# Optimization experiments

Hardware: AMD Instinct MI355X
Metric: run time of the kernel (lower is better)

Reference implementation:

```python
import jax, jax.numpy as jnp
import numpy as np
import math

B, S, D, H, FF, V, L = 8, 1024, 512, 8, 2048, 32000, 6
HD = D // H
EPS = 1e-6


def _positional_encoding(seq_len, d_model):
    pos = np.arange(seq_len, dtype=np.float32)[:, None]
    div = np.exp(np.arange(0, d_model, 2, dtype=np.float32) * (-math.log(10000.0) / d_model))
    pe = np.zeros((seq_len, d_model), dtype=np.float32)
    pe[:, 0::2] = np.sin(pos * div)
    pe[:, 1::2] = np.cos(pos * div)
    return jnp.asarray(pe)[None]  # [1, S, D]


def setup_inputs() -> dict:
    key = jax.random.key(0)
    ks = jax.random.split(key, 10)
    s = 0.02
    return {
        'tokens': jax.random.randint(ks[0], (B, S), 0, V, dtype=jnp.int32),
        'mask': jnp.ones((B, 1, 1, S), dtype=jnp.int32),
        'emb': jax.random.normal(ks[1], (V, D), jnp.float32) * s,
        'Wq': jax.random.normal(ks[2], (D, D), jnp.float32) * s,
        'bq': jnp.zeros((D,), jnp.float32),
        'Wk': jax.random.normal(ks[3], (D, D), jnp.float32) * s,
        'bk': jnp.zeros((D,), jnp.float32),
        'Wv': jax.random.normal(ks[4], (D, D), jnp.float32) * s,
        'bv': jnp.zeros((D,), jnp.float32),
        'Wo': jax.random.normal(ks[5], (D, D), jnp.float32) * s,
        'bo': jnp.zeros((D,), jnp.float32),
        'W1': jax.random.normal(ks[6], (D, FF), jnp.float32) * s,
        'b1': jnp.zeros((FF,), jnp.float32),
        'W2': jax.random.normal(ks[7], (FF, D), jnp.float32) * s,
        'b2': jnp.zeros((D,), jnp.float32),
        'ln_a1': jnp.ones((1,), jnp.float32),
        'ln_b1': jnp.zeros((1,), jnp.float32),
        'ln_a2': jnp.ones((1,), jnp.float32),
        'ln_b2': jnp.zeros((1,), jnp.float32),
    }


def _layernorm(x, alpha, bias):
    # custom LN from source: unbiased std (torch default), scalar alpha/bias,
    # eps added to std (not variance)
    mean = jnp.mean(x, axis=-1, keepdims=True)
    std = jnp.std(x, axis=-1, keepdims=True, ddof=1)
    return alpha * (x - mean) / (std + EPS) + bias


def reference(tokens, mask, emb, Wq, bq, Wk, bk, Wv, bv, Wo, bo,
              W1, b1, W2, b2, ln_a1, ln_b1, ln_a2, ln_b2):
    b, s = tokens.shape
    x = emb[tokens] * jnp.asarray(math.sqrt(D), emb.dtype)  # [B,S,D]
    x = x + _positional_encoding(s, D)
    neg = jnp.asarray(-1e9, x.dtype)
    scale = jnp.asarray(1.0 / math.sqrt(HD), x.dtype)
    # NOTE: source reuses the same EncoderBlock instance -> shared weights per layer
    for _ in range(L):
        # --- self-attention sublayer (pre-norm residual) ---
        h = _layernorm(x, ln_a1, ln_b1)
        q = (h @ Wq + bq).reshape(b, s, H, HD).transpose(0, 2, 1, 3)
        k = (h @ Wk + bk).reshape(b, s, H, HD).transpose(0, 2, 1, 3)
        v = (h @ Wv + bv).reshape(b, s, H, HD).transpose(0, 2, 1, 3)
        scores = jnp.einsum('bhqd,bhkd->bhqk', q, k) * scale
        scores = jnp.where(mask == 0, neg, scores)
        attn = jax.nn.softmax(scores, axis=-1)
        o = jnp.einsum('bhqk,bhkd->bhqd', attn, v)
        o = o.transpose(0, 2, 1, 3).reshape(b, s, D)
        x = x + (o @ Wo + bo)
        # --- feed-forward sublayer (pre-norm residual) ---
        h2 = _layernorm(x, ln_a2, ln_b2)
        x = x + (jax.nn.relu(h2 @ W1 + b1) @ W2 + b2)
    return x
```

## Files before the change

### kernel.cpp

```cpp
#include <hip/hip_runtime.h>
#include <hip/hip_bf16.h>
#include <math.h>

#define BB 8
#define SS 1024
#define DD 512
#define HH 8
#define FF 2048
#define LL 6
#define HD 64
#define MM (BB * SS)
#define EPS 1e-6f
#define QKVS 1536

typedef __attribute__((ext_vector_type(8))) short bf16x8;
typedef __attribute__((ext_vector_type(4))) float f32x4;

typedef __attribute__((address_space(1))) const unsigned int g_u32;
typedef __attribute__((address_space(3))) unsigned int l_u32;

__device__ __forceinline__ short f2bf(float f) {
    union { float f; unsigned u; } c; c.f = f;
    unsigned u = c.u;
    u += 0x7fff + ((u >> 16) & 1);
    return (short)(u >> 16);
}

__device__ __forceinline__ void gload_lds16(const void* g, void* l) {
    __builtin_amdgcn_global_load_lds((g_u32*)g, (l_u32*)l, 16, 0, 0);
}

#define SWZB(row, cb) (((row) * 128) + ((cb) ^ ((((row) & 7) ^ (((row) >> 3) & 7)) << 4)))

__global__ __launch_bounds__(256) void embed_pe_kernel(
    const int* __restrict__ tokens, const float* __restrict__ emb,
    float* __restrict__ x)
{
    int idx = blockIdx.x * 256 + threadIdx.x;
    int d  = idx & (DD - 1);
    int bs = idx >> 9;
    int s  = bs & (SS - 1);
    int tok = tokens[bs];
    float val = emb[(size_t)tok * DD + d] * 22.62741699796952f;
    int i2 = d & ~1;
    float freq = expf((float)i2 * -0.017988946039015984f);
    float ang = (float)s * freq;
    val += (d & 1) ? cosf(ang) : sinf(ang);
    x[idx] = val;
}

__global__ __launch_bounds__(256) void wcvt_kernel(
    const float* __restrict__ W, short* __restrict__ Wt, int K, int N)
{
    __shared__ float tile[32][33];
    int n0 = blockIdx.x * 32, k0 = blockIdx.y * 32;
    int tx = threadIdx.x & 31, ty = threadIdx.x >> 5;
    #pragma unroll
    for (int i = 0; i < 4; ++i)
        tile[ty + i * 8][tx] = W[(size_t)(k0 + ty + i * 8) * N + n0 + tx];
    __syncthreads();
    #pragma unroll
    for (int i = 0; i < 4; ++i)
        Wt[(size_t)(n0 + ty + i * 8) * K + k0 + tx] = f2bf(tile[tx][ty + i * 8]);
}

__global__ __launch_bounds__(256) void bcat_kernel(
    const float* __restrict__ bq, const float* __restrict__ bk,
    const float* __restrict__ bv, float* __restrict__ out)
{
    int i = blockIdx.x * 256 + threadIdx.x;
    float v = (i < 512) ? bq[i] : (i < 1024 ? bk[i - 512] : bv[i - 1024]);
    out[i] = v;
}

__global__ __launch_bounds__(256) void ln_kernel(
    const float* __restrict__ x, short* __restrict__ y,
    const float* __restrict__ alpha_p, const float* __restrict__ beta_p)
{
    int t = threadIdx.x;
    int half = t >> 7, i = t & 127;
    int row = blockIdx.x * 2 + half;
    const float* xr = x + (size_t)row * DD;
    float4 v = *(const float4*)(xr + i * 4);

    __shared__ float red[8];
    float s = v.x + v.y + v.z + v.w;
    #pragma unroll
    for (int o = 32; o >= 1; o >>= 1) s += __shfl_xor(s, o, 64);
    int wv = t >> 6;
    if ((t & 63) == 0) red[wv] = s;
    __syncthreads();
    float mean = (red[half * 2] + red[half * 2 + 1]) * (1.0f / 512.0f);

    float d0 = v.x - mean, d1 = v.y - mean, d2 = v.z - mean, d3 = v.w - mean;
    float q = d0 * d0 + d1 * d1 + d2 * d2 + d3 * d3;
    #pragma unroll
    for (int o = 32; o >= 1; o >>= 1) q += __shfl_xor(q, o, 64);
    if ((t & 63) == 0) red[4 + wv] = q;
    __syncthreads();
    float var = (red[4 + half * 2] + red[5 + half * 2]) * (1.0f / 511.0f);
    float stdv = sqrtf(var);

    float alpha = alpha_p[0], beta = beta_p[0];
    float inv = alpha / (stdv + EPS);
    short4 ov;
    ov.x = f2bf(d0 * inv + beta); ov.y = f2bf(d1 * inv + beta);
    ov.z = f2bf(d2 * inv + beta); ov.w = f2bf(d3 * inv + beta);
    *(short4*)(y + (size_t)row * DD + i * 4) = ov;
}

template <int BN, bool RELU, bool RES, bool OUT_BF16>
__global__ __launch_bounds__(256) void gemm_mfma(
    const short* __restrict__ A, const short* __restrict__ Wt,
    const float* __restrict__ bias, const float* __restrict__ R,
    void* __restrict__ Cout, int M, int N, int K)
{
    __shared__ __align__(16) short As[2][128 * 64];
    __shared__ __align__(16) short Bs[2][BN * 64];

    constexpr int MI = (BN == 128) ? 4 : 2;
    constexpr int NI = 4;

    const int t = threadIdx.x;
    const int w = t >> 6, l = t & 63;
    const int l15 = l & 15, l4 = l >> 4;
    const int wrow = (BN == 128) ? (w >> 1) * 64 : w * 32;
    const int wcol = (BN == 128) ? (w & 1) * 64 : 0;

    const int gx = gridDim.x;
    const int nwg = gx * gridDim.y;
    int id = blockIdx.y * gx + blockIdx.x;
    id = (id & 7) * (nwg >> 3) + (id >> 3);
    const int m0 = (id / gx) * 128, n0 = (id % gx) * BN;

    f32x4 acc[MI][NI];
    #pragma unroll
    for (int mi = 0; mi < MI; ++mi)
        #pragma unroll
        for (int ni = 0; ni < NI; ++ni) acc[mi][ni] = (f32x4){0.f, 0.f, 0.f, 0.f};

    const int lrow = l >> 3;
    const int lcol = (l & 7) * 8;

    auto stage = [&](int bufi, int k0) {
        #pragma unroll
        for (int i = 0; i < 4; ++i) {
            int r0 = (w * 4 + i) * 8;
            gload_lds16(A + (size_t)(m0 + r0 + lrow) * K + k0 + lcol,
                        &As[bufi][r0 * 64]);
        }
        #pragma unroll
        for (int i = 0; i < BN / 32; ++i) {
            int r0 = (w * (BN / 32) + i) * 8;
            gload_lds16(Wt + (size_t)(n0 + r0 + lrow) * K + k0 + lcol,
                        &Bs[bufi][r0 * 64]);
        }
    };

    const int NT = K >> 6;
    stage(0, 0);
    __syncthreads();

    int cur = 0;
    for (int tix = 0; tix < NT; ++tix) {
        if (tix + 1 < NT) stage(cur ^ 1, (tix + 1) * 64);

        #pragma unroll
        for (int ks = 0; ks < 2; ++ks) {
            bf16x8 af[MI], bf_[NI];
            #pragma unroll
            for (int mi = 0; mi < MI; ++mi)
                af[mi] = *(const bf16x8*)&As[cur][(wrow + mi * 16 + l15) * 64 + ks * 32 + l4 * 8];
            #pragma unroll
            for (int ni = 0; ni < NI; ++ni)
                bf_[ni] = *(const bf16x8*)&Bs[cur][(wcol + ni * 16 + l15) * 64 + ks * 32 + l4 * 8];
            #pragma unroll
            for (int mi = 0; mi < MI; ++mi)
                #pragma unroll
                for (int ni = 0; ni < NI; ++ni)
                    acc[mi][ni] = __builtin_amdgcn_mfma_f32_16x16x32_bf16(
                        af[mi], bf_[ni], acc[mi][ni], 0, 0, 0);
        }
        __syncthreads();
        cur ^= 1;
    }

    #pragma unroll
    for (int mi = 0; mi < MI; ++mi) {
        #pragma unroll
        for (int ni = 0; ni < NI; ++ni) {
            int col = n0 + wcol + ni * 16 + l15;
            float bcol = bias[col];
            #pragma unroll
            for (int r = 0; r < 4; ++r) {
                int row = m0 + wrow + mi * 16 + l4 * 4 + r;
                float c = acc[mi][ni][r] + bcol;
                if (RES)  c += R[(size_t)row * N + col];
                if (RELU) c = fmaxf(c, 0.0f);
                if (OUT_BF16) ((short*)Cout)[(size_t)row * N + col] = f2bf(c);
                else          ((float*)Cout)[(size_t)row * N + col] = c;
            }
        }
    }
}

__global__ __launch_bounds__(256) void attn_mfma_kernel(
    const short* __restrict__ qkv, const int* __restrict__ mask,
    short* __restrict__ o)
{
    __shared__ __align__(16) char Ks[64 * 128];
    __shared__ __align__(16) char Vt[64 * 128];
    __shared__ __align__(16) char Ps[4][32 * 128];

    const int qt = blockIdx.x;
    const int bh = blockIdx.y;
    const int b = bh >> 3, h = bh & 7;

    const int t = threadIdx.x;
    const int w = t >> 6;
    const int l = t & 63;
    const int l15 = l & 15, l4 = l >> 4;
    const int l7 = l & 7,  l8 = l >> 3;

    const short* kb = qkv + ((size_t)b * SS) * QKVS + 512 + h * HD;
    const short* vb = qkv + ((size_t)b * SS) * QKVS + 1024 + h * HD;
    const int*   mb = mask + (size_t)b * SS;
    const int qbase = qt * 128 + w * 32;

    bf16x8 qf[2][2];
    #pragma unroll
    for (int qs = 0; qs < 2; ++qs)
        #pragma unroll
        for (int ks = 0; ks < 2; ++ks)
            qf[qs][ks] = *(const bf16x8*)(qkv + ((size_t)b * SS + qbase + qs * 16 + l15) * QKVS
                                          + h * HD + ks * 32 + l4 * 8);

    bf16x8 onesv;
    #pragma unroll
    for (int j = 0; j < 8; ++j) onesv[j] = (short)0x3F80;

    float l_run[2][4];
    f32x4 O[2][4];
    #pragma unroll
    for (int qs = 0; qs < 2; ++qs) {
        #pragma unroll
        for (int r = 0; r < 4; ++r) l_run[qs][r] = 0.0f;
        #pragma unroll
        for (int ds = 0; ds < 4; ++ds) O[qs][ds] = (f32x4){0.f, 0.f, 0.f, 0.f};
    }

    char* Pw = Ps[w];
    const int par = l & 1;
    const int kr = t >> 2;
    const int kc = (t & 3) * 32;

    for (int kt = 0; kt < SS / 64; ++kt) {
        #pragma unroll
        for (int c = 0; c < 2; ++c) {
            bf16x8 kv = *(const bf16x8*)(kb + (size_t)(kt * 64 + kr) * QKVS + (t & 3) * 16 + 8 * c);
            *(bf16x8*)&Ks[SWZB(kr, kc + 16 * c)] = kv;
        }
        #pragma unroll
        for (int s = 0; s < 2; ++s) {
            int key = 16 * w + 8 * s + l7;
            int d0  = 8 * l8;
            int4 vv = *(const int4*)(vb + (size_t)(kt * 64 + key) * QKVS + d0);
            int p0 = __shfl_xor(vv.x, 1, 64);
            int p1 = __shfl_xor(vv.y, 1, 64);
            int p2 = __shfl_xor(vv.z, 1, 64);
            int p3 = __shfl_xor(vv.w, 1, 64);
            int cb = (key & ~1) * 2;
            int v0 = par ? (int)(((unsigned)p0 >> 16) | (vv.x & 0xFFFF0000))
                         : ((vv.x & 0xFFFF) | (p0 << 16));
            int v1 = par ? (int)(((unsigned)p1 >> 16) | (vv.y & 0xFFFF0000))
                         : ((vv.y & 0xFFFF) | (p1 << 16));
            int v2 = par ? (int)(((unsigned)p2 >> 16) | (vv.z & 0xFFFF0000))
                         : ((vv.z & 0xFFFF) | (p2 << 16));
            int v3 = par ? (int)(((unsigned)p3 >> 16) | (vv.w & 0xFFFF0000))
                         : ((vv.w & 0xFFFF) | (p3 << 16));
            *(int*)&Vt[SWZB(d0 + 0 + par, cb)] = v0;
            *(int*)&Vt[SWZB(d0 + 2 + par, cb)] = v1;
            *(int*)&Vt[SWZB(d0 + 4 + par, cb)] = v2;
            *(int*)&Vt[SWZB(d0 + 6 + par, cb)] = v3;
        }
        __syncthreads();

        f32x4 S[2][4];
        #pragma unroll
        for (int qs = 0; qs < 2; ++qs)
            #pragma unroll
            for (int ku = 0; ku < 4; ++ku) S[qs][ku] = (f32x4){0.f, 0.f, 0.f, 0.f};
        __builtin_amdgcn_s_setprio(1);
        #pragma unroll
        for (int ks = 0; ks < 2; ++ks) {
            bf16x8 kf[4];
            #pragma unroll
            for (int ku = 0; ku < 4; ++ku)
                kf[ku] = *(const bf16x8*)&Ks[SWZB(ku * 16 + l15, ks * 64 + l4 * 16)];
            #pragma unroll
            for (int qs = 0; qs < 2; ++qs)
                #pragma unroll
                for (int ku = 0; ku < 4; ++ku)
                    S[qs][ku] = __builtin_amdgcn_mfma_f32_16x16x32_bf16(
                        qf[qs][ks], kf[ku], S[qs][ku], 0, 0, 0);
        }
        __builtin_amdgcn_s_setprio(0);

        int mv[4];
        #pragma unroll
        for (int ku = 0; ku < 4; ++ku) mv[ku] = mb[kt * 64 + ku * 16 + l15];

        #pragma unroll
        for (int qs = 0; qs < 2; ++qs)
            #pragma unroll
            for (int ku = 0; ku < 4; ++ku)
                #pragma unroll
                for (int r = 0; r < 4; ++r) {
                    float sv = (mv[ku] == 0) ? -1e9f : S[qs][ku][r] * 0.125f;
                    *(short*)&Pw[SWZB(qs * 16 + l4 * 4 + r, (ku * 16 + l15) * 2)]
                        = f2bf(__expf(sv));
                }

        __builtin_amdgcn_s_setprio(1);
        #pragma unroll
        for (int qs = 0; qs < 2; ++qs) {
            bf16x8 pf[2];
            #pragma unroll
            for (int ks = 0; ks < 2; ++ks)
                pf[ks] = *(const bf16x8*)&Pw[SWZB(qs * 16 + l15, ks * 64 + l4 * 16)];

            f32x4 rs = (f32x4){0.f, 0.f, 0.f, 0.f};
            rs = __builtin_amdgcn_mfma_f32_16x16x32_bf16(pf[0], onesv, rs, 0, 0, 0);
            rs = __builtin_amdgcn_mfma_f32_16x16x32_bf16(pf[1], onesv, rs, 0, 0, 0);
            #pragma unroll
            for (int r = 0; r < 4; ++r) l_run[qs][r] += rs[r];

            #pragma unroll
            for (int ks = 0; ks < 2; ++ks) {
                bf16x8 vf[4];
                #pragma unroll
                for (int ds = 0; ds < 4; ++ds)
                    vf[ds] = *(const bf16x8*)&Vt[SWZB(ds * 16 + l15, ks * 64 + l4 * 16)];
                #pragma unroll
                for (int ds = 0; ds < 4; ++ds)
                    O[qs][ds] = __builtin_amdgcn_mfma_f32_16x16x32_bf16(
                        pf[ks], vf[ds], O[qs][ds], 0, 0, 0);
            }
        }
        __builtin_amdgcn_s_setprio(0);
        __syncthreads();
    }

    #pragma unroll
    for (int qs = 0; qs < 2; ++qs)
        #pragma unroll
        for (int r = 0; r < 4; ++r) {
            float inv = 1.0f / l_run[qs][r];
            int qrow = qbase + qs * 16 + l4 * 4 + r;
            short* orow = o + ((size_t)b * SS + qrow) * DD + h * HD;
            #pragma unroll
            for (int ds = 0; ds < 4; ++ds)
                orow[ds * 16 + l15] = f2bf(O[qs][ds][r] * inv);
        }
}

extern "C" void kernel_launch(void* const* d_in, const int* in_sizes, int n_in,
                              void* d_out, int out_size, void* d_ws, size_t ws_size,
                              hipStream_t stream)
{
    const int*   tokens = (const int*)  d_in[0];
    const int*   mask   = (const int*)  d_in[1];
    const float* emb    = (const float*)d_in[2];
    const float* Wq     = (const float*)d_in[3];
    const float* bq     = (const float*)d_in[4];
    const float* Wk     = (const float*)d_in[5];
    const float* bk     = (const float*)d_in[6];
    const float* Wv     = (const float*)d_in[7];
    const float* bv     = (const float*)d_in[8];
    const float* Wo     = (const float*)d_in[9];
    const float* bo     = (const float*)d_in[10];
    const float* W1     = (const float*)d_in[11];
    const float* b1     = (const float*)d_in[12];
    const float* W2     = (const float*)d_in[13];
    const float* b2     = (const float*)d_in[14];
    const float* ln_a1  = (const float*)d_in[15];
    const float* ln_b1  = (const float*)d_in[16];
    const float* ln_a2  = (const float*)d_in[17];
    const float* ln_b2  = (const float*)d_in[18];

    float* x = (float*)d_out;

    char* p = (char*)d_ws;
    short* qkv  = (short*)p;  p += (size_t)MM * QKVS * 2;
    short* h    = (short*)p;  p += (size_t)MM * DD * 2;
    short* ff   = (short*)p;  p += (size_t)MM * FF * 2;
    short* Wqkvt= (short*)p;  p += (size_t)QKVS * DD * 2;
    short* Wot  = (short*)p;  p += (size_t)DD * DD * 2;
    short* W1t  = (short*)p;  p += (size_t)FF * DD * 2;
    short* W2t  = (short*)p;  p += (size_t)DD * FF * 2;
    float* bqkv = (float*)p;  p += QKVS * 4;

    embed_pe_kernel<<<(MM * DD) / 256, 256, 0, stream>>>(tokens, emb, x);

    wcvt_kernel<<<dim3(DD / 32, DD / 32), 256, 0, stream>>>(Wq, Wqkvt,            DD, DD);
    wcvt_kernel<<<dim3(DD / 32, DD / 32), 256, 0, stream>>>(Wk, Wqkvt + 512*512,  DD, DD);
    wcvt_kernel<<<dim3(DD / 32, DD / 32), 256, 0, stream>>>(Wv, Wqkvt + 1024*512, DD, DD);
    wcvt_kernel<<<dim3(DD / 32, DD / 32), 256, 0, stream>>>(Wo, Wot, DD, DD);
    wcvt_kernel<<<dim3(FF / 32, DD / 32), 256, 0, stream>>>(W1, W1t, DD, FF);
    wcvt_kernel<<<dim3(DD / 32, FF / 32), 256, 0, stream>>>(W2, W2t, FF, DD);
    bcat_kernel<<<QKVS / 256, 256, 0, stream>>>(bq, bk, bv, bqkv);

    dim3 gQKV(QKVS / 128, MM / 128);
    dim3 gO  (DD / 64,    MM / 128);
    dim3 gF1 (FF / 128,   MM / 128);
    dim3 gF2 (DD / 64,    MM / 128);
    dim3 gA  (SS / 128,   BB * HH);

    for (int layer = 0; layer < LL; ++layer) {
        ln_kernel<<<MM / 2, 256, 0, stream>>>(x, h, ln_a1, ln_b1);
        gemm_mfma<128, false, false, true><<<gQKV, 256, 0, stream>>>(
            h, Wqkvt, bqkv, nullptr, qkv, MM, QKVS, DD);
        attn_mfma_kernel<<<gA, 256, 0, stream>>>(qkv, mask, h);
        gemm_mfma<64, false, true, false><<<gO, 256, 0, stream>>>(
            h, Wot, bo, x, x, MM, DD, DD);

        ln_kernel<<<MM / 2, 256, 0, stream>>>(x, h, ln_a2, ln_b2);
        gemm_mfma<128, true, false, true><<<gF1, 256, 0, stream>>>(
            h, W1t, b1, nullptr, ff, MM, FF, DD);
        gemm_mfma<64, false, true, false><<<gF2, 256, 0, stream>>>(
            ff, W2t, b2, x, x, MM, DD, FF);
    }
}
```

Baseline: 1.237 ms.

## Prefetch next K/V tile into registers in attention and use wave-per-row layernorm

The attention kernel now loads the next 64-key K and V tile from global memory into registers right after the barrier, so those loads overlap with the current tile's MFMA and softmax work instead of stalling at the top of each iteration. The s_setprio hints around the MFMA sections are removed. Layernorm is changed to one wavefront per row with 8 elements per lane, which removes the shared-memory reductions and __syncthreads, and it processes 4 rows per block. The prefetch costs extra registers, which may reduce occupancy in the attention kernel.

```diff
diff --git a/kernel.cpp b/kernel.cpp
--- a/kernel.cpp
+++ b/kernel.cpp
@@ -78,35 +78,33 @@
     const float* __restrict__ alpha_p, const float* __restrict__ beta_p)
 {
     int t = threadIdx.x;
-    int half = t >> 7, i = t & 127;
-    int row = blockIdx.x * 2 + half;
-    const float* xr = x + (size_t)row * DD;
-    float4 v = *(const float4*)(xr + i * 4);
-
-    __shared__ float red[8];
-    float s = v.x + v.y + v.z + v.w;
+    int wv = t >> 6, l = t & 63;
+    int row = blockIdx.x * 4 + wv;
+    const float* xr = x + (size_t)row * DD + l * 8;
+    float4 a = *(const float4*)xr;
+    float4 b = *(const float4*)(xr + 4);
+
+    float v[8] = {a.x, a.y, a.z, a.w, b.x, b.y, b.z, b.w};
+    float s = 0.0f;
+    #pragma unroll
+    for (int j = 0; j < 8; ++j) s += v[j];
     #pragma unroll
     for (int o = 32; o >= 1; o >>= 1) s += __shfl_xor(s, o, 64);
-    int wv = t >> 6;
-    if ((t & 63) == 0) red[wv] = s;
-    __syncthreads();
-    float mean = (red[half * 2] + red[half * 2 + 1]) * (1.0f / 512.0f);
-
-    float d0 = v.x - mean, d1 = v.y - mean, d2 = v.z - mean, d3 = v.w - mean;
-    float q = d0 * d0 + d1 * d1 + d2 * d2 + d3 * d3;
+    float mean = s * (1.0f / 512.0f);
+
+    float q = 0.0f;
+    #pragma unroll
+    for (int j = 0; j < 8; ++j) { v[j] -= mean; q += v[j] * v[j]; }
     #pragma unroll
     for (int o = 32; o >= 1; o >>= 1) q += __shfl_xor(q, o, 64);
-    if ((t & 63) == 0) red[4 + wv] = q;
-    __syncthreads();
-    float var = (red[4 + half * 2] + red[5 + half * 2]) * (1.0f / 511.0f);
-    float stdv = sqrtf(var);
+    float stdv = sqrtf(q * (1.0f / 511.0f));
 
     float alpha = alpha_p[0], beta = beta_p[0];
     float inv = alpha / (stdv + EPS);
-    short4 ov;
-    ov.x = f2bf(d0 * inv + beta); ov.y = f2bf(d1 * inv + beta);
-    ov.z = f2bf(d2 * inv + beta); ov.w = f2bf(d3 * inv + beta);
-    *(short4*)(y + (size_t)row * DD + i * 4) = ov;
+    bf16x8 ov;
+    #pragma unroll
+    for (int j = 0; j < 8; ++j) ov[j] = f2bf(v[j] * inv + beta);
+    *(bf16x8*)(y + (size_t)row * DD + l * 8) = ov;
 }
 
 template <int BN, bool RELU, bool RES, bool OUT_BF16>
@@ -251,20 +249,24 @@
 
     char* Pw = Ps[w];
     const int par = l & 1;
-    const int kr = t >> 2;
-    const int kc = (t & 3) * 32;
+    const int kr  = t >> 2;
+    const int kcs = (t & 3) * 16;
+    const int vkey0 = 16 * w + l7;
+    const int vkey1 = 16 * w + 8 + l7;
+    const int vd0 = 8 * l8;
+
+    bf16x8 kreg0 = *(const bf16x8*)(kb + (size_t)kr * QKVS + kcs);
+    bf16x8 kreg1 = *(const bf16x8*)(kb + (size_t)kr * QKVS + kcs + 8);
+    int4   vreg0 = *(const int4*)(vb + (size_t)vkey0 * QKVS + vd0);
+    int4   vreg1 = *(const int4*)(vb + (size_t)vkey1 * QKVS + vd0);
 
     for (int kt = 0; kt < SS / 64; ++kt) {
-        #pragma unroll
-        for (int c = 0; c < 2; ++c) {
-            bf16x8 kv = *(const bf16x8*)(kb + (size_t)(kt * 64 + kr) * QKVS + (t & 3) * 16 + 8 * c);
-            *(bf16x8*)&Ks[SWZB(kr, kc + 16 * c)] = kv;
-        }
+        *(bf16x8*)&Ks[SWZB(kr, kcs * 2)]      = kreg0;
+        *(bf16x8*)&Ks[SWZB(kr, kcs * 2 + 16)] = kreg1;
         #pragma unroll
         for (int s = 0; s < 2; ++s) {
-            int key = 16 * w + 8 * s + l7;
-            int d0  = 8 * l8;
-            int4 vv = *(const int4*)(vb + (size_t)(kt * 64 + key) * QKVS + d0);
+            int4 vv = s ? vreg1 : vreg0;
+            int key = s ? vkey1 : vkey0;
             int p0 = __shfl_xor(vv.x, 1, 64);
             int p1 = __shfl_xor(vv.y, 1, 64);
             int p2 = __shfl_xor(vv.z, 1, 64);
@@ -278,19 +280,27 @@
                          : ((vv.z & 0xFFFF) | (p2 << 16));
             int v3 = par ? (int)(((unsigned)p3 >> 16) | (vv.w & 0xFFFF0000))
                          : ((vv.w & 0xFFFF) | (p3 << 16));
-            *(int*)&Vt[SWZB(d0 + 0 + par, cb)] = v0;
-            *(int*)&Vt[SWZB(d0 + 2 + par, cb)] = v1;
-            *(int*)&Vt[SWZB(d0 + 4 + par, cb)] = v2;
-            *(int*)&Vt[SWZB(d0 + 6 + par, cb)] = v3;
+            *(int*)&Vt[SWZB(vd0 + 0 + par, cb)] = v0;
+            *(int*)&Vt[SWZB(vd0 + 2 + par, cb)] = v1;
+            *(int*)&Vt[SWZB(vd0 + 4 + par, cb)] = v2;
+            *(int*)&Vt[SWZB(vd0 + 6 + par, cb)] = v3;
         }
         __syncthreads();
 
+        if (kt + 1 < SS / 64) {
+            const short* kbn = kb + (size_t)((kt + 1) * 64) * QKVS;
+            const short* vbn = vb + (size_t)((kt + 1) * 64) * QKVS;
+            kreg0 = *(const bf16x8*)(kbn + (size_t)kr * QKVS + kcs);
+            kreg1 = *(const bf16x8*)(kbn + (size_t)kr * QKVS + kcs + 8);
+            vreg0 = *(const int4*)(vbn + (size_t)vkey0 * QKVS + vd0);
+            vreg1 = *(const int4*)(vbn + (size_t)vkey1 * QKVS + vd0);
+        }
+
         f32x4 S[2][4];
         #pragma unroll
         for (int qs = 0; qs < 2; ++qs)
             #pragma unroll
             for (int ku = 0; ku < 4; ++ku) S[qs][ku] = (f32x4){0.f, 0.f, 0.f, 0.f};
-        __builtin_amdgcn_s_setprio(1);
         #pragma unroll
         for (int ks = 0; ks < 2; ++ks) {
             bf16x8 kf[4];
@@ -304,7 +314,6 @@
                     S[qs][ku] = __builtin_amdgcn_mfma_f32_16x16x32_bf16(
                         qf[qs][ks], kf[ku], S[qs][ku], 0, 0, 0);
         }
-        __builtin_amdgcn_s_setprio(0);
 
         int mv[4];
         #pragma unroll
@@ -321,7 +330,6 @@
                         = f2bf(__expf(sv));
                 }
 
-        __builtin_amdgcn_s_setprio(1);
         #pragma unroll
         for (int qs = 0; qs < 2; ++qs) {
             bf16x8 pf[2];
@@ -347,7 +355,6 @@
                         pf[ks], vf[ds], O[qs][ds], 0, 0, 0);
             }
         }
-        __builtin_amdgcn_s_setprio(0);
         __syncthreads();
     }
 
@@ -417,14 +424,14 @@
     dim3 gA  (SS / 128,   BB * HH);
 
     for (int layer = 0; layer < LL; ++layer) {
-        ln_kernel<<<MM / 2, 256, 0, stream>>>(x, h, ln_a1, ln_b1);
+        ln_kernel<<<MM / 4, 256, 0, stream>>>(x, h, ln_a1, ln_b1);
         gemm_mfma<128, false, false, true><<<gQKV, 256, 0, stream>>>(
             h, Wqkvt, bqkv, nullptr, qkv, MM, QKVS, DD);
         attn_mfma_kernel<<<gA, 256, 0, stream>>>(qkv, mask, h);
         gemm_mfma<64, false, true, false><<<gO, 256, 0, stream>>>(
             h, Wot, bo, x, x, MM, DD, DD);
 
-        ln_kernel<<<MM / 2, 256, 0, stream>>>(x, h, ln_a2, ln_b2);
+        ln_kernel<<<MM / 4, 256, 0, stream>>>(x, h, ln_a2, ln_b2);
         gemm_mfma<128, true, false, true><<<gF1, 256, 0, stream>>>(
             h, W1t, b1, nullptr, ff, MM, FF, DD);
         gemm_mfma<64, false, true, false><<<gF2, 256, 0, stream>>>(
```

New measurement: 1.199 ms. 1.03x faster.
